# Kernel optimization log

Measured on AMD Instinct MI355X. Metric: run time of the kernel, lower is better.

## Reference

```python
import jax, jax.numpy as jnp
import numpy as np

H, D = 6, 64          # num_heads, head_dim (embed_dim = 384)
WIN = 33              # window_size
PAD = (WIN - 1) // 2  # 16


def setup_inputs() -> dict:
    key = jax.random.key(0)
    ks = jax.random.split(key, 9)
    B, L, E = 8, 1025, 384
    s = 1.0 / np.sqrt(E).astype(np.float32)
    return {
        "x": jax.random.normal(ks[0], (B, L, E), jnp.float32),
        "Wq": jax.random.normal(ks[1], (E, E), jnp.float32) * s,
        "bq": jax.random.normal(ks[2], (E,), jnp.float32) * 0.01,
        "Wk": jax.random.normal(ks[3], (E, E), jnp.float32) * s,
        "bk": jax.random.normal(ks[4], (E,), jnp.float32) * 0.01,
        "Wv": jax.random.normal(ks[5], (E, E), jnp.float32) * s,
        "bv": jax.random.normal(ks[6], (E,), jnp.float32) * 0.01,
        "Wo": jax.random.normal(ks[7], (E, E), jnp.float32) * s,
        "bo": jax.random.normal(ks[8], (E,), jnp.float32) * 0.01,
    }


def reference(x, Wq, bq, Wk, bk, Wv, bv, Wo, bo):
    B, L, E = x.shape
    scale = 1.0 / np.sqrt(D).astype(np.float32)

    def proj(W, b):
        # (B,L,E) -> (B,H,L,D)
        return (x @ W + b).reshape(B, L, H, D).transpose(0, 2, 1, 3)

    Q, K, V = proj(Wq, bq), proj(Wk, bk), proj(Wv, bv)

    # --- cls token (position 0): full attention over all keys ---
    s_cls = jnp.einsum('bhqd,bhkd->bhqk', Q[:, :, :1], K) * scale
    out_cls = jnp.einsum('bhqk,bhkd->bhqd', jax.nn.softmax(s_cls, -1), V)

    # --- remaining tokens: local window + cls appended to every window ---
    Lr = L - 1
    pos = jnp.arange(1, L)                                    # absolute query pos (Lr,)
    idx = pos[:, None] + jnp.arange(WIN)[None, :] - PAD
    # original masks out-of-range AND the cls slot (abs pos 0) inside the window
    valid = (idx >= 1) & (idx < L)
    idxc = jnp.clip(idx, 0, L - 1)

    Kw = K[:, :, idxc]
    Vw = V[:, :, idxc]
    cls_k = jnp.broadcast_to(K[:, :, :1, None, :], (B, H, Lr, 1, D))
    cls_v = jnp.broadcast_to(V[:, :, :1, None, :], (B, H, Lr, 1, D))
    Kw = jnp.concatenate([Kw, cls_k], axis=3)
    Vw = jnp.concatenate([Vw, cls_v], axis=3)
    mask = jnp.concatenate([valid, jnp.ones((Lr, 1), bool)], axis=-1)

    s_rest = jnp.einsum('bhld,bhlwd->bhlw', Q[:, :, 1:], Kw) * scale
    s_rest = jnp.where(mask[None, None], s_rest, -jnp.inf)
    a_rest = jax.nn.softmax(s_rest, axis=-1)
    out_rest = jnp.einsum('bhlw,bhlwd->bhld', a_rest, Vw)

    out = jnp.concatenate([out_cls, out_rest], axis=2)        # (B,H,L,D)
    out = out.transpose(0, 2, 1, 3).reshape(B, L, E)
    return out @ Wo + bo
```

## Files before the change

kernel.cpp:

```cpp
#include <hip/hip_runtime.h>
#include <hip/hip_bf16.h>

typedef unsigned short ushort_t;
typedef __attribute__((ext_vector_type(8))) short short8;
typedef __attribute__((ext_vector_type(4))) float f32x4;

constexpr int Bc = 8;
constexpr int Lc = 1025;
constexpr int Ec = 384;
constexpr int Hc = 6;
constexpr int Dc = 64;
constexpr int MT = Bc * Lc;
constexpr int BHLD = Bc * Hc * Lc * Dc;
constexpr float SCALE = 0.125f;
constexpr int NCH = 5;

__device__ __forceinline__ float bf2f(ushort_t u) {
    union { unsigned int u; float f; } v; v.u = ((unsigned int)u) << 16; return v.f;
}
__device__ __forceinline__ ushort_t f2bf(float f) {
    union { float f; unsigned int u; } v; v.f = f;
    unsigned int r = v.u + 0x7FFFu + ((v.u >> 16) & 1u);
    return (ushort_t)(r >> 16);
}

#define GLOAD_LDS16(gp, lp)                                                          \
    __builtin_amdgcn_global_load_lds(                                                \
        (const __attribute__((address_space(1))) unsigned int*)(gp),                 \
        (__attribute__((address_space(3))) unsigned int*)(lp), 16, 0, 0)

__global__ __launch_bounds__(256) void prep_kernel(
    const float* __restrict__ x, ushort_t* __restrict__ xb,
    const float* __restrict__ Wq, const float* __restrict__ Wk,
    const float* __restrict__ Wv, const float* __restrict__ Wo,
    ushort_t* __restrict__ Wt_all)
{
    const int bid = blockIdx.x;
    if (bid < 3075) {
        int i = bid * 256 + threadIdx.x;
        float4 v = ((const float4*)x)[i];
        ushort4 o;
        o.x = f2bf(v.x); o.y = f2bf(v.y); o.z = f2bf(v.z); o.w = f2bf(v.w);
        ((ushort4*)xb)[i] = o;
        return;
    }
    __shared__ float t[32][33];
    const int b2 = bid - 3075;
    const int z = b2 / 144, rem = b2 - z * 144;
    const int yy = rem / 12, xx = rem - yy * 12;
    const float* W = (z == 0) ? Wq : (z == 1) ? Wk : (z == 2) ? Wv : Wo;
    ushort_t* Wt = Wt_all + (size_t)z * Ec * Ec;
    const int x0 = xx * 32, y0 = yy * 32;
    const int tx = threadIdx.x & 31, ty = threadIdx.x >> 5;
#pragma unroll
    for (int j = 0; j < 4; j++)
        t[ty + 8 * j][tx] = W[(size_t)(y0 + ty + 8 * j) * Ec + x0 + tx];
    __syncthreads();
#pragma unroll
    for (int j = 0; j < 4; j++)
        Wt[(size_t)(x0 + ty + 8 * j) * Ec + y0 + tx] = f2bf(t[tx][ty + 8 * j]);
}

__global__ __launch_bounds__(256) void qkv_mfma_kernel(
    const ushort_t* __restrict__ xb, const ushort_t* __restrict__ Wt,
    const float* __restrict__ bq, const float* __restrict__ bk,
    const float* __restrict__ bv, ushort_t* __restrict__ qkv)
{
    __shared__ __align__(16) ushort_t Asm[64 * 384];
    __shared__ __align__(16) ushort_t Bsm[2][128 * 64];

    const int tid = threadIdx.x;
    const int lane = tid & 63;
    const int wid = tid >> 6;
    const int wr = wid & 1, wc = wid >> 1;
    const int m0 = blockIdx.x * 64;
    const int which = blockIdx.y;
    const ushort_t* Wmat = Wt + (size_t)which * Ec * Ec;
    const float* bias = (which == 0) ? bq : (which == 1) ? bk : bv;
    ushort_t* outp = qkv + (size_t)which * BHLD;

#pragma unroll
    for (int i = 0; i < 12; i++) {
        int wchunk = wid * 12 + i;
        int ci = wchunk * 64 + lane;
        int row = ci / 48, c = ci - row * 48;
        int cg = (c & ~7) | ((c & 7) ^ (row & 7));
        int rowA = m0 + row; rowA = rowA < MT ? rowA : MT - 1;
        GLOAD_LDS16(xb + (size_t)rowA * Ec + cg * 8,
                    Asm + (size_t)wchunk * 512);
    }

#define B_STAGE(S, BUF)                                                          \
    {                                                                            \
        int ns_ = (S) / 6, kt_ = (S) - ns_ * 6;                                  \
        _Pragma("unroll")                                                        \
        for (int c = 0; c < 4; c++) {                                            \
            int ci  = (wid * 4 + c) * 64 + lane;                                 \
            int row = ci >> 3, kc = ci & 7;                                      \
            int kcs = kc ^ (row & 7);                                            \
            GLOAD_LDS16(Wmat + (size_t)(ns_ * 128 + row) * Ec + kt_ * 64 + kcs * 8, \
                        Bsm[BUF] + (size_t)(wid * 4 + c) * 512);                 \
        }                                                                        \
    }

    B_STAGE(0, 0);
    B_STAGE(1, 1);

    f32x4 acc[2][4];
#pragma unroll
    for (int i = 0; i < 2; i++)
#pragma unroll
        for (int j = 0; j < 4; j++) acc[i][j] = (f32x4){0.f, 0.f, 0.f, 0.f};

    const int colL = lane & 15;
    const int rowL = (lane >> 4) * 4;

    for (int s = 0; s < 18; ++s) {
        const int cb = s & 1;
        const int ns = s / 6, kt = s - ns * 6;
        if (s < 17) { asm volatile("s_waitcnt vmcnt(4)" ::: "memory"); }
        else        { asm volatile("s_waitcnt vmcnt(0)" ::: "memory"); }
        __builtin_amdgcn_sched_barrier(0);
        __builtin_amdgcn_s_barrier();

        short8 a[2][2], b[2][4];
#pragma unroll
        for (int ki = 0; ki < 2; ki++) {
            const int kc = ki * 4 + (lane >> 4);
#pragma unroll
            for (int mi = 0; mi < 2; mi++) {
                int row = wr * 32 + mi * 16 + (lane & 15);
                a[ki][mi] = *(const short8*)(
                    Asm + row * 384 + (kt * 8 + (kc ^ (row & 7))) * 8);
            }
#pragma unroll
            for (int ni = 0; ni < 4; ni++) {
                int row = wc * 64 + ni * 16 + (lane & 15);
                b[ki][ni] = *(const short8*)(
                    Bsm[cb] + row * 64 + ((kc ^ (row & 7)) * 8));
            }
        }
        asm volatile("s_waitcnt lgkmcnt(0)" ::: "memory");
        __builtin_amdgcn_sched_barrier(0);
        __builtin_amdgcn_s_barrier();

        if (s + 2 < 18) B_STAGE(s + 2, cb);

#pragma unroll
        for (int ki = 0; ki < 2; ki++)
#pragma unroll
            for (int mi = 0; mi < 2; mi++)
#pragma unroll
                for (int ni = 0; ni < 4; ni++)
                    acc[mi][ni] = __builtin_amdgcn_mfma_f32_16x16x32_bf16(
                        a[ki][mi], b[ki][ni], acc[mi][ni], 0, 0, 0);

        if (kt == 5) {
#pragma unroll
            for (int ni = 0; ni < 4; ni++) {
                int nm = ns * 128 + wc * 64 + ni * 16 + colL;
                float bv_ = bias[nm];
                int h = nm >> 6, d = nm & 63;
#pragma unroll
                for (int mi = 0; mi < 2; mi++) {
#pragma unroll
                    for (int r = 0; r < 4; r++) {
                        int m = m0 + wr * 32 + mi * 16 + rowL + r;
                        if (m < MT) {
                            int b_ = m / Lc, l = m - b_ * Lc;
                            outp[((size_t)(b_ * Hc + h) * Lc + l) * Dc + d] =
                                f2bf(acc[mi][ni][r] + bv_);
                        }
                    }
                    acc[mi][ni] = (f32x4){0.f, 0.f, 0.f, 0.f};
                }
            }
        }
    }
#undef B_STAGE
}

__global__ __launch_bounds__(256) void cls_part_kernel(
    const ushort_t* __restrict__ qkv, float* __restrict__ part)
{
    const int bh = blockIdx.x, ch = blockIdx.y;
    const int base = ch * 256;
    const int count = min(256, Lc - base);
    const ushort_t* Q = qkv + (size_t)bh * Lc * Dc;
    const ushort_t* K = Q + (size_t)BHLD;
    const ushort_t* V = Q + 2 * (size_t)BHLD;

    __shared__ float qs[64];
    __shared__ float ps[256];
    __shared__ float red[256];

    const int tid = threadIdx.x;
    if (tid < 64) qs[tid] = bf2f(Q[tid]);
    __syncthreads();

    float s = -1e30f;
    if (tid < count) {
        const ushort4* kp = (const ushort4*)(K + (size_t)(base + tid) * Dc);
        float acc = 0.f;
#pragma unroll
        for (int c = 0; c < 16; c++) {
            ushort4 kv = kp[c];
            acc += qs[c * 4 + 0] * bf2f(kv.x) + qs[c * 4 + 1] * bf2f(kv.y) +
                   qs[c * 4 + 2] * bf2f(kv.z) + qs[c * 4 + 3] * bf2f(kv.w);
        }
        s = acc * SCALE;
    }
    red[tid] = s; __syncthreads();
    for (int off = 128; off > 0; off >>= 1) {
        if (tid < off) red[tid] = fmaxf(red[tid], red[tid + off]);
        __syncthreads();
    }
    const float m = red[0];
    __syncthreads();

    float p = (tid < count) ? __expf(s - m) : 0.f;
    ps[tid] = p;
    red[tid] = p; __syncthreads();
    for (int off = 128; off > 0; off >>= 1) {
        if (tid < off) red[tid] += red[tid + off];
        __syncthreads();
    }
    const float S = red[0];
    __syncthreads();

    const int d = tid & 63, sl = tid >> 6;
    float acc = 0.f;
    for (int i = sl; i < count; i += 4)
        acc += ps[i] * bf2f(V[(size_t)(base + i) * Dc + d]);
    red[tid] = acc; __syncthreads();
    if (tid < 64) {
        float o = red[tid] + red[tid + 64] + red[tid + 128] + red[tid + 192];
        float* pp = part + (size_t)(bh * NCH + ch) * 66;
        pp[2 + tid] = o;
        if (tid == 0) { pp[0] = m; pp[1] = S; }
    }
}

__global__ __launch_bounds__(256) void win_attn_kernel(
    const ushort_t* __restrict__ qkv, const float* __restrict__ part,
    ushort_t* __restrict__ attnb)
{
    __shared__ __align__(16) ushort_t Kb[128 * 64];
    __shared__ __align__(16) ushort_t Vb[64 * 128];
    __shared__ __align__(16) ushort_t QP[64 * 128];

    const int bh = blockIdx.y;
    const int tid = threadIdx.x, lane = tid & 63, wid = tid >> 6;
    const int b_ = bh / Hc, h = bh - b_ * Hc;

    if (blockIdx.x == 16) {
        if (tid >= 64) return;
        float M = -1e30f;
#pragma unroll
        for (int ch = 0; ch < NCH; ch++)
            M = fmaxf(M, part[(size_t)(bh * NCH + ch) * 66]);
        float S = 0.f, O = 0.f;
#pragma unroll
        for (int ch = 0; ch < NCH; ch++) {
            const float* pp = part + (size_t)(bh * NCH + ch) * 66;
            float w = __expf(pp[0] - M);
            S += pp[1] * w;
            O += pp[2 + tid] * w;
        }
        attnb[(size_t)(b_ * Lc) * Ec + h * 64 + tid] = f2bf(O / S);
        return;
    }

    const int t = blockIdx.x;
    const int l0 = 1 + t * 64;
    const int k0n = l0 - 16;
    const ushort_t* Qg = qkv + (size_t)bh * Lc * Dc;
    const ushort_t* Kg = Qg + (size_t)BHLD;
    const ushort_t* Vg = Qg + 2 * (size_t)BHLD;

    short8 vreg[4];
    int vrow[4], vdc[4];
#pragma unroll
    for (int i = 0; i < 4; i++) {
        int ci = i * 256 + tid;
        if (ci < 896) {
            int j = ci >> 3, dc = ci & 7;
            int kp = (j <= 95) ? min(max(k0n + j, 0), 1024) : 0;
            vreg[i] = *(const short8*)(Vg + (size_t)kp * Dc + dc * 8);
            vrow[i] = j; vdc[i] = dc;
        } else { vrow[i] = -1; vdc[i] = 0; }
    }

#pragma unroll
    for (int i = 0; i < 4; i++) {
        int wchunk = i * 4 + wid;
        if (wchunk < 14) {
            int p = wchunk * 64 + lane;
            int j = p >> 3, c = p & 7, g = c ^ (j & 7);
            int kp = (j <= 95) ? min(max(k0n + j, 0), 1024) : 0;
            GLOAD_LDS16(Kg + (size_t)kp * Dc + g * 8,
                        Kb + (size_t)wchunk * 512);
        }
    }
#pragma unroll
    for (int i = 0; i < 2; i++) {
        int p = (i * 4 + wid) * 64 + lane;
        int q = p >> 3, c = p & 7, g = c ^ (q & 7);
        GLOAD_LDS16(Qg + (size_t)(l0 + q) * Dc + g * 8,
                    QP + (size_t)(i * 4 + wid) * 512);
    }

#pragma unroll
    for (int i = 0; i < 4; i++) {
        if (vrow[i] >= 0) {
            int j = vrow[i], jc3 = j >> 3, j7 = j & 7;
#pragma unroll
            for (int z = 0; z < 8; z++) {
                int d = vdc[i] * 8 + z;
                Vb[d * 128 + ((jc3 ^ (d & 15)) * 8) + j7] = (ushort_t)vreg[i][z];
            }
        }
    }
    if (tid < 128) {
        int d = tid >> 1, lcn = 14 + (tid & 1);
        *(short8*)(Vb + d * 128 + ((lcn ^ (d & 15)) * 8)) =
            (short8){0, 0, 0, 0, 0, 0, 0, 0};
    }
    __syncthreads();

    f32x4 sacc[7];
#pragma unroll
    for (int tj = 0; tj < 7; tj++) sacc[tj] = (f32x4){0.f, 0.f, 0.f, 0.f};
#pragma unroll
    for (int ki = 0; ki < 2; ki++) {
        const int gc = ki * 4 + (lane >> 4);
        const int qrow = wid * 16 + (lane & 15);
        short8 a = *(const short8*)(QP + qrow * 64 + ((gc ^ (qrow & 7)) * 8));
#pragma unroll
        for (int tj = 0; tj < 7; tj++) {
            int jrow = tj * 16 + (lane & 15);
            short8 b = *(const short8*)(Kb + jrow * 64 + ((gc ^ (jrow & 7)) * 8));
            sacc[tj] = __builtin_amdgcn_mfma_f32_16x16x32_bf16(a, b, sacc[tj], 0, 0, 0);
        }
    }
    __syncthreads();

    const int qb = wid * 16 + (lane >> 4) * 4;
    const int cl = lane & 15;
    float inv[4];
#pragma unroll
    for (int r = 0; r < 4; r++) {
        const int q = qb + r;
        float sv[7];
        float mx = -1e30f;
#pragma unroll
        for (int tj = 0; tj < 7; tj++) {
            int j = tj * 16 + cl;
            int kp = k0n + j;
            bool valid = (j == 96) ||
                         ((j >= q) && (j <= q + 32) && (kp >= 1) && (kp <= 1024));
            float s = valid ? sacc[tj][r] * SCALE : -1e30f;
            sv[tj] = s;
            mx = fmaxf(mx, s);
        }
        mx = fmaxf(mx, __shfl_xor(mx, 1));
        mx = fmaxf(mx, __shfl_xor(mx, 2));
        mx = fmaxf(mx, __shfl_xor(mx, 4));
        mx = fmaxf(mx, __shfl_xor(mx, 8));
        float sum = 0.f;
#pragma unroll
        for (int tj = 0; tj < 7; tj++) {
            float pv = __expf(sv[tj] - mx);
            sv[tj] = pv;
            sum += pv;
        }
        sum += __shfl_xor(sum, 1);
        sum += __shfl_xor(sum, 2);
        sum += __shfl_xor(sum, 4);
        sum += __shfl_xor(sum, 8);
        inv[r] = 1.f / sum;
#pragma unroll
        for (int tj = 0; tj < 7; tj++) {
            int j = tj * 16 + cl;
            QP[q * 128 + (((j >> 3) ^ (q & 15)) * 8) + (j & 7)] = f2bf(sv[tj]);
        }
    }
    if (cl == 0) {
#pragma unroll
        for (int r = 0; r < 4; r++) {
            int q = qb + r;
            *(short8*)(QP + q * 128 + ((14 ^ (q & 15)) * 8)) =
                (short8){0, 0, 0, 0, 0, 0, 0, 0};
            *(short8*)(QP + q * 128 + ((15 ^ (q & 15)) * 8)) =
                (short8){0, 0, 0, 0, 0, 0, 0, 0};
        }
    }
    __syncthreads();

    f32x4 oacc[4];
#pragma unroll
    for (int dt = 0; dt < 4; dt++) oacc[dt] = (f32x4){0.f, 0.f, 0.f, 0.f};
#pragma unroll
    for (int kc = 0; kc < 4; kc++) {
        const int gc = kc * 4 + (lane >> 4);
        const int qrow = wid * 16 + (lane & 15);
        short8 pa = *(const short8*)(QP + qrow * 128 + ((gc ^ (qrow & 15)) * 8));
#pragma unroll
        for (int dt = 0; dt < 4; dt++) {
            int drow = dt * 16 + (lane & 15);
            short8 vb = *(const short8*)(Vb + drow * 128 + ((gc ^ (drow & 15)) * 8));
            oacc[dt] = __builtin_amdgcn_mfma_f32_16x16x32_bf16(pa, vb, oacc[dt], 0, 0, 0);
        }
    }

#pragma unroll
    for (int dt = 0; dt < 4; dt++) {
        int d = dt * 16 + cl;
#pragma unroll
        for (int r = 0; r < 4; r++) {
            int l = l0 + qb + r;
            attnb[(size_t)(b_ * Lc + l) * Ec + h * 64 + d] = f2bf(oacc[dt][r] * inv[r]);
        }
    }
}

__global__ __launch_bounds__(256) void out_mfma_kernel(
    const ushort_t* __restrict__ attn_rows, const ushort_t* __restrict__ Wot,
    const float* __restrict__ bo, float* __restrict__ out)
{
    __shared__ __align__(16) ushort_t As[2][64 * 64];
    __shared__ __align__(16) ushort_t Bs[2][128 * 64];

    const int tid = threadIdx.x;
    const int lane = tid & 63;
    const int wid = tid >> 6;
    const int wr = wid & 1, wc = wid >> 1;
    const int m0 = blockIdx.x * 64;
    const int n0 = blockIdx.y * 128;

    f32x4 acc[2][4];
#pragma unroll
    for (int i = 0; i < 2; i++)
#pragma unroll
        for (int j = 0; j < 4; j++) acc[i][j] = (f32x4){0.f, 0.f, 0.f, 0.f};

#define OUT_STAGE(KT, BUF)                                                       \
    {                                                                            \
        _Pragma("unroll")                                                        \
        for (int c = 0; c < 2; c++) {                                            \
            int ci  = (wid * 2 + c) * 64 + lane;                                 \
            int row = ci >> 3, kc = ci & 7;                                      \
            int kcs = kc ^ (row & 7);                                            \
            int rowA = m0 + row; rowA = rowA < MT ? rowA : MT - 1;               \
            GLOAD_LDS16(attn_rows + (size_t)rowA * Ec + (KT) + kcs * 8,          \
                        As[BUF] + (size_t)(wid * 2 + c) * 512);                  \
        }                                                                        \
        _Pragma("unroll")                                                        \
        for (int c = 0; c < 4; c++) {                                            \
            int ci  = (wid * 4 + c) * 64 + lane;                                 \
            int row = ci >> 3, kc = ci & 7;                                      \
            int kcs = kc ^ (row & 7);                                            \
            GLOAD_LDS16(Wot + (size_t)(n0 + row) * Ec + (KT) + kcs * 8,          \
                        Bs[BUF] + (size_t)(wid * 4 + c) * 512);                  \
        }                                                                        \
    }

    OUT_STAGE(0, 0);
    OUT_STAGE(64, 1);

    for (int t = 0; t < 6; ++t) {
        const int cb = t & 1;
        if (t < 5) { asm volatile("s_waitcnt vmcnt(6)" ::: "memory"); }
        else       { asm volatile("s_waitcnt vmcnt(0)" ::: "memory"); }
        __builtin_amdgcn_sched_barrier(0);
        __builtin_amdgcn_s_barrier();

        short8 a[2][2], b[2][4];
#pragma unroll
        for (int ki = 0; ki < 2; ki++) {
            const int kchunk = ki * 4 + (lane >> 4);
#pragma unroll
            for (int mi = 0; mi < 2; mi++) {
                int row = wr * 32 + mi * 16 + (lane & 15);
                a[ki][mi] = *(const short8*)(As[cb] + row * 64 + ((kchunk ^ (row & 7)) * 8));
            }
#pragma unroll
            for (int ni = 0; ni < 4; ni++) {
                int row = wc * 64 + ni * 16 + (lane & 15);
                b[ki][ni] = *(const short8*)(Bs[cb] + row * 64 + ((kchunk ^ (row & 7)) * 8));
            }
        }
        asm volatile("s_waitcnt lgkmcnt(0)" ::: "memory");
        __builtin_amdgcn_sched_barrier(0);
        __builtin_amdgcn_s_barrier();

        if (t + 2 < 6) OUT_STAGE((t + 2) * 64, cb);

#pragma unroll
        for (int ki = 0; ki < 2; ki++)
#pragma unroll
            for (int mi = 0; mi < 2; mi++)
#pragma unroll
                for (int ni = 0; ni < 4; ni++)
                    acc[mi][ni] = __builtin_amdgcn_mfma_f32_16x16x32_bf16(
                        a[ki][mi], b[ki][ni], acc[mi][ni], 0, 0, 0);
    }
#undef OUT_STAGE

    const int colL = lane & 15;
    const int rowL = (lane >> 4) * 4;
#pragma unroll
    for (int ni = 0; ni < 4; ni++) {
        int n = n0 + wc * 64 + ni * 16 + colL;
        float bo_v = bo[n];
#pragma unroll
        for (int mi = 0; mi < 2; mi++) {
#pragma unroll
            for (int r = 0; r < 4; r++) {
                int m = m0 + wr * 32 + mi * 16 + rowL + r;
                if (m < MT) out[(size_t)m * Ec + n] = acc[mi][ni][r] + bo_v;
            }
        }
    }
}

extern "C" void kernel_launch(void* const* d_in, const int* in_sizes, int n_in,
                              void* d_out, int out_size, void* d_ws, size_t ws_size,
                              hipStream_t stream)
{
    const float* x  = (const float*)d_in[0];
    const float* Wq = (const float*)d_in[1];
    const float* bq = (const float*)d_in[2];
    const float* Wk = (const float*)d_in[3];
    const float* bk = (const float*)d_in[4];
    const float* Wv = (const float*)d_in[5];
    const float* bv = (const float*)d_in[6];
    const float* Wo = (const float*)d_in[7];
    const float* bo = (const float*)d_in[8];
    float* out = (float*)d_out;

    ushort_t* xb    = (ushort_t*)d_ws;
    ushort_t* Wt    = xb + (size_t)MT * Ec;
    ushort_t* qkvb  = Wt + (size_t)4 * Ec * Ec;
    ushort_t* attnb = qkvb + (size_t)3 * BHLD;
    float* clsp     = (float*)(attnb + (size_t)MT * Ec);

    prep_kernel<<<3075 + 576, 256, 0, stream>>>(x, xb, Wq, Wk, Wv, Wo, Wt);

    qkv_mfma_kernel<<<dim3((MT + 63) / 64, 3), 256, 0, stream>>>(
        xb, Wt, bq, bk, bv, qkvb);

    cls_part_kernel<<<dim3(Bc * Hc, NCH), 256, 0, stream>>>(qkvb, clsp);

    win_attn_kernel<<<dim3(17, Bc * Hc), 256, 0, stream>>>(qkvb, clsp, attnb);

    out_mfma_kernel<<<dim3((MT + 63) / 64, 3), 256, 0, stream>>>(
        attnb, Wt + (size_t)3 * Ec * Ec, bo, out);
}
```

Baseline: 160.3 us.

## Fuse all stages into one persistent cooperative kernel with grid syncs

Replaces five separate kernel launches (prep, QKV GEMM, cls partials, window attention, output GEMM) with one cooperative persistent kernel that walks each stage's jobs in a grid-stride loop and separates stages with grid.sync(). Shared memory comes from one 80 KB pool that each stage reinterprets. The aim is to remove launch gaps and per-kernel tail effects. In exchange, grid-wide barriers add cost, the grid is capped at 512 blocks, and the large LDS pool and register pressure may limit occupancy for the GEMM and attention phases.

```diff
diff --git a/kernel.cpp b/kernel.cpp
--- a/kernel.cpp
+++ b/kernel.cpp
@@ -1,5 +1,8 @@
 #include <hip/hip_runtime.h>
 #include <hip/hip_bf16.h>
+#include <hip/hip_cooperative_groups.h>
+
+namespace cg = cooperative_groups;
 
 typedef unsigned short ushort_t;
 typedef __attribute__((ext_vector_type(8))) short short8;
@@ -29,66 +32,74 @@
         (const __attribute__((address_space(1))) unsigned int*)(gp),                 \
         (__attribute__((address_space(3))) unsigned int*)(lp), 16, 0, 0)
 
-__global__ __launch_bounds__(256) void prep_kernel(
-    const float* __restrict__ x, ushort_t* __restrict__ xb,
+__global__ __launch_bounds__(256, 2) void fused_kernel(
+    const float* __restrict__ x,
     const float* __restrict__ Wq, const float* __restrict__ Wk,
     const float* __restrict__ Wv, const float* __restrict__ Wo,
-    ushort_t* __restrict__ Wt_all)
+    const float* __restrict__ bq, const float* __restrict__ bk,
+    const float* __restrict__ bv, const float* __restrict__ bo,
+    ushort_t* __restrict__ xb, ushort_t* __restrict__ Wt_all,
+    ushort_t* __restrict__ qkvb, float* __restrict__ clsp,
+    ushort_t* __restrict__ attnb, float* __restrict__ out)
 {
-    const int bid = blockIdx.x;
-    if (bid < 3075) {
-        int i = bid * 256 + threadIdx.x;
-        float4 v = ((const float4*)x)[i];
-        ushort4 o;
-        o.x = f2bf(v.x); o.y = f2bf(v.y); o.z = f2bf(v.z); o.w = f2bf(v.w);
-        ((ushort4*)xb)[i] = o;
-        return;
-    }
-    __shared__ float t[32][33];
-    const int b2 = bid - 3075;
-    const int z = b2 / 144, rem = b2 - z * 144;
-    const int yy = rem / 12, xx = rem - yy * 12;
-    const float* W = (z == 0) ? Wq : (z == 1) ? Wk : (z == 2) ? Wv : Wo;
-    ushort_t* Wt = Wt_all + (size_t)z * Ec * Ec;
-    const int x0 = xx * 32, y0 = yy * 32;
-    const int tx = threadIdx.x & 31, ty = threadIdx.x >> 5;
-#pragma unroll
-    for (int j = 0; j < 4; j++)
-        t[ty + 8 * j][tx] = W[(size_t)(y0 + ty + 8 * j) * Ec + x0 + tx];
-    __syncthreads();
-#pragma unroll
-    for (int j = 0; j < 4; j++)
-        Wt[(size_t)(x0 + ty + 8 * j) * Ec + y0 + tx] = f2bf(t[tx][ty + 8 * j]);
-}
-
-__global__ __launch_bounds__(256) void qkv_mfma_kernel(
-    const ushort_t* __restrict__ xb, const ushort_t* __restrict__ Wt,
-    const float* __restrict__ bq, const float* __restrict__ bk,
-    const float* __restrict__ bv, ushort_t* __restrict__ qkv)
-{
-    __shared__ __align__(16) ushort_t Asm[64 * 384];
-    __shared__ __align__(16) ushort_t Bsm[2][128 * 64];
-
+    __shared__ __align__(16) unsigned char POOL[81920];
+
+    cg::grid_group grid = cg::this_grid();
+    const int nb  = gridDim.x;
+    const int bx  = blockIdx.x;
     const int tid = threadIdx.x;
     const int lane = tid & 63;
-    const int wid = tid >> 6;
-    const int wr = wid & 1, wc = wid >> 1;
-    const int m0 = blockIdx.x * 64;
-    const int which = blockIdx.y;
-    const ushort_t* Wmat = Wt + (size_t)which * Ec * Ec;
-    const float* bias = (which == 0) ? bq : (which == 1) ? bk : bv;
-    ushort_t* outp = qkv + (size_t)which * BHLD;
-
-#pragma unroll
-    for (int i = 0; i < 12; i++) {
-        int wchunk = wid * 12 + i;
-        int ci = wchunk * 64 + lane;
-        int row = ci / 48, c = ci - row * 48;
-        int cg = (c & ~7) | ((c & 7) ^ (row & 7));
-        int rowA = m0 + row; rowA = rowA < MT ? rowA : MT - 1;
-        GLOAD_LDS16(xb + (size_t)rowA * Ec + cg * 8,
-                    Asm + (size_t)wchunk * 512);
-    }
+    const int wid  = tid >> 6;
+
+    for (int job = bx; job < 3075 + 576; job += nb) {
+        if (job < 3075) {
+            int i = job * 256 + tid;
+            float4 v = ((const float4*)x)[i];
+            ushort4 o;
+            o.x = f2bf(v.x); o.y = f2bf(v.y); o.z = f2bf(v.z); o.w = f2bf(v.w);
+            ((ushort4*)xb)[i] = o;
+        } else {
+            float (*t)[33] = (float (*)[33])POOL;
+            const int b2 = job - 3075;
+            const int z = b2 / 144, rem = b2 - z * 144;
+            const int yy = rem / 12, xx = rem - yy * 12;
+            const float* W = (z == 0) ? Wq : (z == 1) ? Wk : (z == 2) ? Wv : Wo;
+            ushort_t* Wt = Wt_all + (size_t)z * Ec * Ec;
+            const int x0 = xx * 32, y0 = yy * 32;
+            const int tx = tid & 31, ty = tid >> 5;
+#pragma unroll
+            for (int j = 0; j < 4; j++)
+                t[ty + 8 * j][tx] = W[(size_t)(y0 + ty + 8 * j) * Ec + x0 + tx];
+            __syncthreads();
+#pragma unroll
+            for (int j = 0; j < 4; j++)
+                Wt[(size_t)(x0 + ty + 8 * j) * Ec + y0 + tx] = f2bf(t[tx][ty + 8 * j]);
+            __syncthreads();
+        }
+    }
+    grid.sync();
+
+    for (int job = bx; job < 129 * 3; job += nb) {
+        ushort_t* Asm = (ushort_t*)POOL;
+        ushort_t* BsmB = (ushort_t*)(POOL + 49152);
+
+        const int wr = wid & 1, wc = wid >> 1;
+        const int m0 = (job % 129) * 64;
+        const int which = job / 129;
+        const ushort_t* Wmat = Wt_all + (size_t)which * Ec * Ec;
+        const float* bias = (which == 0) ? bq : (which == 1) ? bk : bv;
+        ushort_t* outp = qkvb + (size_t)which * BHLD;
+
+#pragma unroll
+        for (int i = 0; i < 12; i++) {
+            int wchunk = wid * 12 + i;
+            int ci = wchunk * 64 + lane;
+            int row = ci / 48, c = ci - row * 48;
+            int cg_ = (c & ~7) | ((c & 7) ^ (row & 7));
+            int rowA = m0 + row; rowA = rowA < MT ? rowA : MT - 1;
+            GLOAD_LDS16(xb + (size_t)rowA * Ec + cg_ * 8,
+                        Asm + (size_t)wchunk * 512);
+        }
 
 #define B_STAGE(S, BUF)                                                          \
     {                                                                            \
@@ -99,350 +110,345 @@
             int row = ci >> 3, kc = ci & 7;                                      \
             int kcs = kc ^ (row & 7);                                            \
             GLOAD_LDS16(Wmat + (size_t)(ns_ * 128 + row) * Ec + kt_ * 64 + kcs * 8, \
-                        Bsm[BUF] + (size_t)(wid * 4 + c) * 512);                 \
+                        BsmB + (size_t)(BUF) * 8192 + (size_t)(wid * 4 + c) * 512); \
         }                                                                        \
     }
 
-    B_STAGE(0, 0);
-    B_STAGE(1, 1);
-
-    f32x4 acc[2][4];
-#pragma unroll
-    for (int i = 0; i < 2; i++)
-#pragma unroll
-        for (int j = 0; j < 4; j++) acc[i][j] = (f32x4){0.f, 0.f, 0.f, 0.f};
-
-    const int colL = lane & 15;
-    const int rowL = (lane >> 4) * 4;
-
-    for (int s = 0; s < 18; ++s) {
-        const int cb = s & 1;
-        const int ns = s / 6, kt = s - ns * 6;
-        if (s < 17) { asm volatile("s_waitcnt vmcnt(4)" ::: "memory"); }
-        else        { asm volatile("s_waitcnt vmcnt(0)" ::: "memory"); }
-        __builtin_amdgcn_sched_barrier(0);
-        __builtin_amdgcn_s_barrier();
-
-        short8 a[2][2], b[2][4];
+        B_STAGE(0, 0);
+        B_STAGE(1, 1);
+
+        f32x4 acc[2][4];
+#pragma unroll
+        for (int i = 0; i < 2; i++)
+#pragma unroll
+            for (int j = 0; j < 4; j++) acc[i][j] = (f32x4){0.f, 0.f, 0.f, 0.f};
+
+        const int colL = lane & 15;
+        const int rowL = (lane >> 4) * 4;
+
+        for (int s = 0; s < 18; ++s) {
+            const int cb = s & 1;
+            const int ns = s / 6, kt = s - ns * 6;
+            if (s < 17) { asm volatile("s_waitcnt vmcnt(4)" ::: "memory"); }
+            else        { asm volatile("s_waitcnt vmcnt(0)" ::: "memory"); }
+            __builtin_amdgcn_sched_barrier(0);
+            __builtin_amdgcn_s_barrier();
+
+            short8 a[2][2], b[2][4];
+#pragma unroll
+            for (int ki = 0; ki < 2; ki++) {
+                const int kc = ki * 4 + (lane >> 4);
+#pragma unroll
+                for (int mi = 0; mi < 2; mi++) {
+                    int row = wr * 32 + mi * 16 + (lane & 15);
+                    a[ki][mi] = *(const short8*)(
+                        Asm + row * 384 + (kt * 8 + (kc ^ (row & 7))) * 8);
+                }
+#pragma unroll
+                for (int ni = 0; ni < 4; ni++) {
+                    int row = wc * 64 + ni * 16 + (lane & 15);
+                    b[ki][ni] = *(const short8*)(
+                        BsmB + (size_t)cb * 8192 + row * 64 + ((kc ^ (row & 7)) * 8));
+                }
+            }
+            asm volatile("s_waitcnt lgkmcnt(0)" ::: "memory");
+            __builtin_amdgcn_sched_barrier(0);
+            __builtin_amdgcn_s_barrier();
+
+            if (s + 2 < 18) B_STAGE(s + 2, cb);
+
+#pragma unroll
+            for (int ki = 0; ki < 2; ki++)
+#pragma unroll
+                for (int mi = 0; mi < 2; mi++)
+#pragma unroll
+                    for (int ni = 0; ni < 4; ni++)
+                        acc[mi][ni] = __builtin_amdgcn_mfma_f32_16x16x32_bf16(
+                            a[ki][mi], b[ki][ni], acc[mi][ni], 0, 0, 0);
+
+            if (kt == 5) {
+#pragma unroll
+                for (int ni = 0; ni < 4; ni++) {
+                    int nm = ns * 128 + wc * 64 + ni * 16 + colL;
+                    float bv_ = bias[nm];
+                    int h = nm >> 6, d = nm & 63;
+#pragma unroll
+                    for (int mi = 0; mi < 2; mi++) {
+#pragma unroll
+                        for (int r = 0; r < 4; r++) {
+                            int m = m0 + wr * 32 + mi * 16 + rowL + r;
+                            if (m < MT) {
+                                int b_ = m / Lc, l = m - b_ * Lc;
+                                outp[((size_t)(b_ * Hc + h) * Lc + l) * Dc + d] =
+                                    f2bf(acc[mi][ni][r] + bv_);
+                            }
+                        }
+                        acc[mi][ni] = (f32x4){0.f, 0.f, 0.f, 0.f};
+                    }
+                }
+            }
+        }
+#undef B_STAGE
+    }
+    grid.sync();
+
+    for (int job = bx; job < Bc * Hc * NCH; job += nb) {
+        float* qs  = (float*)POOL;
+        float* ps  = qs + 64;
+        float* red = ps + 256;
+
+        const int bh = job / NCH, ch = job - bh * NCH;
+        const int base = ch * 256;
+        const int count = min(256, Lc - base);
+        const ushort_t* Q = qkvb + (size_t)bh * Lc * Dc;
+        const ushort_t* K = Q + (size_t)BHLD;
+        const ushort_t* V = Q + 2 * (size_t)BHLD;
+
+        if (tid < 64) qs[tid] = bf2f(Q[tid]);
+        __syncthreads();
+
+        float s = -1e30f;
+        if (tid < count) {
+            const ushort4* kp = (const ushort4*)(K + (size_t)(base + tid) * Dc);
+            float acc = 0.f;
+#pragma unroll
+            for (int c = 0; c < 16; c++) {
+                ushort4 kv = kp[c];
+                acc += qs[c * 4 + 0] * bf2f(kv.x) + qs[c * 4 + 1] * bf2f(kv.y) +
+                       qs[c * 4 + 2] * bf2f(kv.z) + qs[c * 4 + 3] * bf2f(kv.w);
+            }
+            s = acc * SCALE;
+        }
+        red[tid] = s; __syncthreads();
+        for (int off = 128; off > 0; off >>= 1) {
+            if (tid < off) red[tid] = fmaxf(red[tid], red[tid + off]);
+            __syncthreads();
+        }
+        const float m = red[0];
+        __syncthreads();
+
+        float p = (tid < count) ? __expf(s - m) : 0.f;
+        ps[tid] = p;
+        red[tid] = p; __syncthreads();
+        for (int off = 128; off > 0; off >>= 1) {
+            if (tid < off) red[tid] += red[tid + off];
+            __syncthreads();
+        }
+        const float S = red[0];
+        __syncthreads();
+
+        const int d = tid & 63, sl = tid >> 6;
+        float acc = 0.f;
+        for (int i = sl; i < count; i += 4)
+            acc += ps[i] * bf2f(V[(size_t)(base + i) * Dc + d]);
+        red[tid] = acc; __syncthreads();
+        if (tid < 64) {
+            float o = red[tid] + red[tid + 64] + red[tid + 128] + red[tid + 192];
+            float* pp = clsp + (size_t)(bh * NCH + ch) * 66;
+            pp[2 + tid] = o;
+            if (tid == 0) { pp[0] = m; pp[1] = S; }
+        }
+        __syncthreads();
+    }
+    grid.sync();
+
+    for (int job = bx; job < 768 + 48; job += nb) {
+        __syncthreads();
+
+        if (job >= 768) {
+            const int bh = job - 768;
+            const int b_ = bh / Hc, h = bh - b_ * Hc;
+            if (tid < 64) {
+                float M = -1e30f;
+#pragma unroll
+                for (int ch = 0; ch < NCH; ch++)
+                    M = fmaxf(M, clsp[(size_t)(bh * NCH + ch) * 66]);
+                float S = 0.f, O = 0.f;
+#pragma unroll
+                for (int ch = 0; ch < NCH; ch++) {
+                    const float* pp = clsp + (size_t)(bh * NCH + ch) * 66;
+                    float w = __expf(pp[0] - M);
+                    S += pp[1] * w;
+                    O += pp[2 + tid] * w;
+                }
+                attnb[(size_t)(b_ * Lc) * Ec + h * 64 + tid] = f2bf(O / S);
+            }
+            continue;
+        }
+
+        ushort_t* Kb = (ushort_t*)POOL;
+        ushort_t* Vb = (ushort_t*)(POOL + 16384);
+        ushort_t* QP = (ushort_t*)(POOL + 32768);
+
+        const int t = job % 16, bh = job / 16;
+        const int b_ = bh / Hc, h = bh - b_ * Hc;
+        const int l0 = 1 + t * 64;
+        const int k0n = l0 - 16;
+        const ushort_t* Qg = qkvb + (size_t)bh * Lc * Dc;
+        const ushort_t* Kg = Qg + (size_t)BHLD;
+        const ushort_t* Vg = Qg + 2 * (size_t)BHLD;
+
+        short8 vreg[4];
+        int vrow[4], vdc[4];
+#pragma unroll
+        for (int i = 0; i < 4; i++) {
+            int ci = i * 256 + tid;
+            if (ci < 896) {
+                int j = ci >> 3, dc = ci & 7;
+                int kp = (j <= 95) ? min(max(k0n + j, 0), 1024) : 0;
+                vreg[i] = *(const short8*)(Vg + (size_t)kp * Dc + dc * 8);
+                vrow[i] = j; vdc[i] = dc;
+            } else { vrow[i] = -1; vdc[i] = 0; }
+        }
+
+#pragma unroll
+        for (int i = 0; i < 4; i++) {
+            int wchunk = i * 4 + wid;
+            if (wchunk < 14) {
+                int p = wchunk * 64 + lane;
+                int j = p >> 3, c = p & 7, g = c ^ (j & 7);
+                int kp = (j <= 95) ? min(max(k0n + j, 0), 1024) : 0;
+                GLOAD_LDS16(Kg + (size_t)kp * Dc + g * 8,
+                            Kb + (size_t)wchunk * 512);
+            }
+        }
+#pragma unroll
+        for (int i = 0; i < 2; i++) {
+            int p = (i * 4 + wid) * 64 + lane;
+            int q = p >> 3, c = p & 7, g = c ^ (q & 7);
+            GLOAD_LDS16(Qg + (size_t)(l0 + q) * Dc + g * 8,
+                        QP + (size_t)(i * 4 + wid) * 512);
+        }
+
+#pragma unroll
+        for (int i = 0; i < 4; i++) {
+            if (vrow[i] >= 0) {
+                int j = vrow[i], jc3 = j >> 3, j7 = j & 7;
+#pragma unroll
+                for (int z = 0; z < 8; z++) {
+                    int d = vdc[i] * 8 + z;
+                    Vb[d * 128 + ((jc3 ^ (d & 15)) * 8) + j7] = (ushort_t)vreg[i][z];
+                }
+            }
+        }
+        if (tid < 128) {
+            int d = tid >> 1, lcn = 14 + (tid & 1);
+            *(short8*)(Vb + d * 128 + ((lcn ^ (d & 15)) * 8)) =
+                (short8){0, 0, 0, 0, 0, 0, 0, 0};
+        }
+        __syncthreads();
+
+        f32x4 sacc[7];
+#pragma unroll
+        for (int tj = 0; tj < 7; tj++) sacc[tj] = (f32x4){0.f, 0.f, 0.f, 0.f};
 #pragma unroll
         for (int ki = 0; ki < 2; ki++) {
-            const int kc = ki * 4 + (lane >> 4);
-#pragma unroll
-            for (int mi = 0; mi < 2; mi++) {
-                int row = wr * 32 + mi * 16 + (lane & 15);
-                a[ki][mi] = *(const short8*)(
-                    Asm + row * 384 + (kt * 8 + (kc ^ (row & 7))) * 8);
-            }
-#pragma unroll
-            for (int ni = 0; ni < 4; ni++) {
-                int row = wc * 64 + ni * 16 + (lane & 15);
-                b[ki][ni] = *(const short8*)(
-                    Bsm[cb] + row * 64 + ((kc ^ (row & 7)) * 8));
-            }
-        }
-        asm volatile("s_waitcnt lgkmcnt(0)" ::: "memory");
-        __builtin_amdgcn_sched_barrier(0);
-        __builtin_amdgcn_s_barrier();
-
-        if (s + 2 < 18) B_STAGE(s + 2, cb);
-
-#pragma unroll
-        for (int ki = 0; ki < 2; ki++)
-#pragma unroll
-            for (int mi = 0; mi < 2; mi++)
-#pragma unroll
-                for (int ni = 0; ni < 4; ni++)
-                    acc[mi][ni] = __builtin_amdgcn_mfma_f32_16x16x32_bf16(
-                        a[ki][mi], b[ki][ni], acc[mi][ni], 0, 0, 0);
-
-        if (kt == 5) {
-#pragma unroll
-            for (int ni = 0; ni < 4; ni++) {
-                int nm = ns * 128 + wc * 64 + ni * 16 + colL;
-                float bv_ = bias[nm];
-                int h = nm >> 6, d = nm & 63;
-#pragma unroll
-                for (int mi = 0; mi < 2; mi++) {
-#pragma unroll
-                    for (int r = 0; r < 4; r++) {
-                        int m = m0 + wr * 32 + mi * 16 + rowL + r;
-                        if (m < MT) {
-                            int b_ = m / Lc, l = m - b_ * Lc;
-                            outp[((size_t)(b_ * Hc + h) * Lc + l) * Dc + d] =
-                                f2bf(acc[mi][ni][r] + bv_);
-                        }
-                    }
-                    acc[mi][ni] = (f32x4){0.f, 0.f, 0.f, 0.f};
-                }
-            }
-        }
-    }
-#undef B_STAGE
-}
-
-__global__ __launch_bounds__(256) void cls_part_kernel(
-    const ushort_t* __restrict__ qkv, float* __restrict__ part)
-{
-    const int bh = blockIdx.x, ch = blockIdx.y;
-    const int base = ch * 256;
-    const int count = min(256, Lc - base);
-    const ushort_t* Q = qkv + (size_t)bh * Lc * Dc;
-    const ushort_t* K = Q + (size_t)BHLD;
-    const ushort_t* V = Q + 2 * (size_t)BHLD;
-
-    __shared__ float qs[64];
-    __shared__ float ps[256];
-    __shared__ float red[256];
-
-    const int tid = threadIdx.x;
-    if (tid < 64) qs[tid] = bf2f(Q[tid]);
-    __syncthreads();
-
-    float s = -1e30f;
-    if (tid < count) {
-        const ushort4* kp = (const ushort4*)(K + (size_t)(base + tid) * Dc);
-        float acc = 0.f;
-#pragma unroll
-        for (int c = 0; c < 16; c++) {
-            ushort4 kv = kp[c];
-            acc += qs[c * 4 + 0] * bf2f(kv.x) + qs[c * 4 + 1] * bf2f(kv.y) +
-                   qs[c * 4 + 2] * bf2f(kv.z) + qs[c * 4 + 3] * bf2f(kv.w);
-        }
-        s = acc * SCALE;
-    }
-    red[tid] = s; __syncthreads();
-    for (int off = 128; off > 0; off >>= 1) {
-        if (tid < off) red[tid] = fmaxf(red[tid], red[tid + off]);
-        __syncthreads();
-    }
-    const float m = red[0];
-    __syncthreads();
-
-    float p = (tid < count) ? __expf(s - m) : 0.f;
-    ps[tid] = p;
-    red[tid] = p; __syncthreads();
-    for (int off = 128; off > 0; off >>= 1) {
-        if (tid < off) red[tid] += red[tid + off];
-        __syncthreads();
-    }
-    const float S = red[0];
-    __syncthreads();
-
-    const int d = tid & 63, sl = tid >> 6;
-    float acc = 0.f;
-    for (int i = sl; i < count; i += 4)
-        acc += ps[i] * bf2f(V[(size_t)(base + i) * Dc + d]);
-    red[tid] = acc; __syncthreads();
-    if (tid < 64) {
-        float o = red[tid] + red[tid + 64] + red[tid + 128] + red[tid + 192];
-        float* pp = part + (size_t)(bh * NCH + ch) * 66;
-        pp[2 + tid] = o;
-        if (tid == 0) { pp[0] = m; pp[1] = S; }
-    }
-}
-
-__global__ __launch_bounds__(256) void win_attn_kernel(
-    const ushort_t* __restrict__ qkv, const float* __restrict__ part,
-    ushort_t* __restrict__ attnb)
-{
-    __shared__ __align__(16) ushort_t Kb[128 * 64];
-    __shared__ __align__(16) ushort_t Vb[64 * 128];
-    __shared__ __align__(16) ushort_t QP[64 * 128];
-
-    const int bh = blockIdx.y;
-    const int tid = threadIdx.x, lane = tid & 63, wid = tid >> 6;
-    const int b_ = bh / Hc, h = bh - b_ * Hc;
-
-    if (blockIdx.x == 16) {
-        if (tid >= 64) return;
-        float M = -1e30f;
-#pragma unroll
-        for (int ch = 0; ch < NCH; ch++)
-            M = fmaxf(M, part[(size_t)(bh * NCH + ch) * 66]);
-        float S = 0.f, O = 0.f;
-#pragma unroll
-        for (int ch = 0; ch < NCH; ch++) {
-            const float* pp = part + (size_t)(bh * NCH + ch) * 66;
-            float w = __expf(pp[0] - M);
-            S += pp[1] * w;
-            O += pp[2 + tid] * w;
-        }
-        attnb[(size_t)(b_ * Lc) * Ec + h * 64 + tid] = f2bf(O / S);
-        return;
-    }
-
-    const int t = blockIdx.x;
-    const int l0 = 1 + t * 64;
-    const int k0n = l0 - 16;
-    const ushort_t* Qg = qkv + (size_t)bh * Lc * Dc;
-    const ushort_t* Kg = Qg + (size_t)BHLD;
-    const ushort_t* Vg = Qg + 2 * (size_t)BHLD;
-
-    short8 vreg[4];
-    int vrow[4], vdc[4];
-#pragma unroll
-    for (int i = 0; i < 4; i++) {
-        int ci = i * 256 + tid;
-        if (ci < 896) {
-            int j = ci >> 3, dc = ci & 7;
-            int kp = (j <= 95) ? min(max(k0n + j, 0), 1024) : 0;
-            vreg[i] = *(const short8*)(Vg + (size_t)kp * Dc + dc * 8);
-            vrow[i] = j; vdc[i] = dc;
-        } else { vrow[i] = -1; vdc[i] = 0; }
-    }
-
-#pragma unroll
-    for (int i = 0; i < 4; i++) {
-        int wchunk = i * 4 + wid;
-        if (wchunk < 14) {
-            int p = wchunk * 64 + lane;
-            int j = p >> 3, c = p & 7, g = c ^ (j & 7);
-            int kp = (j <= 95) ? min(max(k0n + j, 0), 1024) : 0;
-            GLOAD_LDS16(Kg + (size_t)kp * Dc + g * 8,
-                        Kb + (size_t)wchunk * 512);
-        }
-    }
-#pragma unroll
-    for (int i = 0; i < 2; i++) {
-        int p = (i * 4 + wid) * 64 + lane;
-        int q = p >> 3, c = p & 7, g = c ^ (q & 7);
-        GLOAD_LDS16(Qg + (size_t)(l0 + q) * Dc + g * 8,
-                    QP + (size_t)(i * 4 + wid) * 512);
-    }
-
-#pragma unroll
-    for (int i = 0; i < 4; i++) {
-        if (vrow[i] >= 0) {
-            int j = vrow[i], jc3 = j >> 3, j7 = j & 7;
-#pragma unroll
-            for (int z = 0; z < 8; z++) {
-                int d = vdc[i] * 8 + z;
-                Vb[d * 128 + ((jc3 ^ (d & 15)) * 8) + j7] = (ushort_t)vreg[i][z];
-            }
-        }
-    }
-    if (tid < 128) {
-        int d = tid >> 1, lcn = 14 + (tid & 1);
-        *(short8*)(Vb + d * 128 + ((lcn ^ (d & 15)) * 8)) =
-            (short8){0, 0, 0, 0, 0, 0, 0, 0};
-    }
-    __syncthreads();
-
-    f32x4 sacc[7];
-#pragma unroll
-    for (int tj = 0; tj < 7; tj++) sacc[tj] = (f32x4){0.f, 0.f, 0.f, 0.f};
-#pragma unroll
-    for (int ki = 0; ki < 2; ki++) {
-        const int gc = ki * 4 + (lane >> 4);
-        const int qrow = wid * 16 + (lane & 15);
-        short8 a = *(const short8*)(QP + qrow * 64 + ((gc ^ (qrow & 7)) * 8));
-#pragma unroll
-        for (int tj = 0; tj < 7; tj++) {
-            int jrow = tj * 16 + (lane & 15);
-            short8 b = *(const short8*)(Kb + jrow * 64 + ((gc ^ (jrow & 7)) * 8));
-            sacc[tj] = __builtin_amdgcn_mfma_f32_16x16x32_bf16(a, b, sacc[tj], 0, 0, 0);
-        }
-    }
-    __syncthreads();
-
-    const int qb = wid * 16 + (lane >> 4) * 4;
-    const int cl = lane & 15;
-    float inv[4];
-#pragma unroll
-    for (int r = 0; r < 4; r++) {
-        const int q = qb + r;
-        float sv[7];
-        float mx = -1e30f;
-#pragma unroll
-        for (int tj = 0; tj < 7; tj++) {
-            int j = tj * 16 + cl;
-            int kp = k0n + j;
-            bool valid = (j == 96) ||
-                         ((j >= q) && (j <= q + 32) && (kp >= 1) && (kp <= 1024));
-            float s = valid ? sacc[tj][r] * SCALE : -1e30f;
-            sv[tj] = s;
-            mx = fmaxf(mx, s);
-        }
-        mx = fmaxf(mx, __shfl_xor(mx, 1));
-        mx = fmaxf(mx, __shfl_xor(mx, 2));
-        mx = fmaxf(mx, __shfl_xor(mx, 4));
-        mx = fmaxf(mx, __shfl_xor(mx, 8));
-        float sum = 0.f;
-#pragma unroll
-        for (int tj = 0; tj < 7; tj++) {
-            float pv = __expf(sv[tj] - mx);
-            sv[tj] = pv;
-            sum += pv;
-        }
-        sum += __shfl_xor(sum, 1);
-        sum += __shfl_xor(sum, 2);
-        sum += __shfl_xor(sum, 4);
-        sum += __shfl_xor(sum, 8);
-        inv[r] = 1.f / sum;
-#pragma unroll
-        for (int tj = 0; tj < 7; tj++) {
-            int j = tj * 16 + cl;
-            QP[q * 128 + (((j >> 3) ^ (q & 15)) * 8) + (j & 7)] = f2bf(sv[tj]);
-        }
-    }
-    if (cl == 0) {
+            const int gc = ki * 4 + (lane >> 4);
+            const int qrow = wid * 16 + (lane & 15);
+            short8 a = *(const short8*)(QP + qrow * 64 + ((gc ^ (qrow & 7)) * 8));
+#pragma unroll
+            for (int tj = 0; tj < 7; tj++) {
+                int jrow = tj * 16 + (lane & 15);
+                short8 b = *(const short8*)(Kb + jrow * 64 + ((gc ^ (jrow & 7)) * 8));
+                sacc[tj] = __builtin_amdgcn_mfma_f32_16x16x32_bf16(a, b, sacc[tj], 0, 0, 0);
+            }
+        }
+        __syncthreads();
+
+        const int qb = wid * 16 + (lane >> 4) * 4;
+        const int cl = lane & 15;
+        float inv[4];
 #pragma unroll
         for (int r = 0; r < 4; r++) {
-            int q = qb + r;
-            *(short8*)(QP + q * 128 + ((14 ^ (q & 15)) * 8)) =
-                (short8){0, 0, 0, 0, 0, 0, 0, 0};
-            *(short8*)(QP + q * 128 + ((15 ^ (q & 15)) * 8)) =
-                (short8){0, 0, 0, 0, 0, 0, 0, 0};
-        }
-    }
-    __syncthreads();
-
-    f32x4 oacc[4];
-#pragma unroll
-    for (int dt = 0; dt < 4; dt++) oacc[dt] = (f32x4){0.f, 0.f, 0.f, 0.f};
-#pragma unroll
-    for (int kc = 0; kc < 4; kc++) {
-        const int gc = kc * 4 + (lane >> 4);
-        const int qrow = wid * 16 + (lane & 15);
-        short8 pa = *(const short8*)(QP + qrow * 128 + ((gc ^ (qrow & 15)) * 8));
+            const int q = qb + r;
+            float sv[7];
+            float mx = -1e30f;
+#pragma unroll
+            for (int tj = 0; tj < 7; tj++) {
+                int j = tj * 16 + cl;
+                int kp = k0n + j;
+                bool valid = (j == 96) ||
+                             ((j >= q) && (j <= q + 32) && (kp >= 1) && (kp <= 1024));
+                float s = valid ? sacc[tj][r] * SCALE : -1e30f;
+                sv[tj] = s;
+                mx = fmaxf(mx, s);
+            }
+            mx = fmaxf(mx, __shfl_xor(mx, 1));
+            mx = fmaxf(mx, __shfl_xor(mx, 2));
+            mx = fmaxf(mx, __shfl_xor(mx, 4));
+            mx = fmaxf(mx, __shfl_xor(mx, 8));
+            float sum = 0.f;
+#pragma unroll
+            for (int tj = 0; tj < 7; tj++) {
+                float pv = __expf(sv[tj] - mx);
+                sv[tj] = pv;
+                sum += pv;
+            }
+            sum += __shfl_xor(sum, 1);
+            sum += __shfl_xor(sum, 2);
+            sum += __shfl_xor(sum, 4);
+            sum += __shfl_xor(sum, 8);
+            inv[r] = 1.f / sum;
+#pragma unroll
+            for (int tj = 0; tj < 7; tj++) {
+                int j = tj * 16 + cl;
+                QP[q * 128 + (((j >> 3) ^ (q & 15)) * 8) + (j & 7)] = f2bf(sv[tj]);
+            }
+        }
+        if (cl == 0) {
+#pragma unroll
+            for (int r = 0; r < 4; r++) {
+                int q = qb + r;
+                *(short8*)(QP + q * 128 + ((14 ^ (q & 15)) * 8)) =
+                    (short8){0, 0, 0, 0, 0, 0, 0, 0};
+                *(short8*)(QP + q * 128 + ((15 ^ (q & 15)) * 8)) =
+                    (short8){0, 0, 0, 0, 0, 0, 0, 0};
+            }
+        }
+        __syncthreads();
+
+        f32x4 oacc[4];
+#pragma unroll
+        for (int dt = 0; dt < 4; dt++) oacc[dt] = (f32x4){0.f, 0.f, 0.f, 0.f};
+#pragma unroll
+        for (int kc = 0; kc < 4; kc++) {
+            const int gc = kc * 4 + (lane >> 4);
+            const int qrow = wid * 16 + (lane & 15);
+            short8 pa = *(const short8*)(QP + qrow * 128 + ((gc ^ (qrow & 15)) * 8));
+#pragma unroll
+            for (int dt = 0; dt < 4; dt++) {
+                int drow = dt * 16 + (lane & 15);
+                short8 vb = *(const short8*)(Vb + drow * 128 + ((gc ^ (drow & 15)) * 8));
+                oacc[dt] = __builtin_amdgcn_mfma_f32_16x16x32_bf16(pa, vb, oacc[dt], 0, 0, 0);
+            }
+        }
+
 #pragma unroll
         for (int dt = 0; dt < 4; dt++) {
-            int drow = dt * 16 + (lane & 15);
-            short8 vb = *(const short8*)(Vb + drow * 128 + ((gc ^ (drow & 15)) * 8));
-            oacc[dt] = __builtin_amdgcn_mfma_f32_16x16x32_bf16(pa, vb, oacc[dt], 0, 0, 0);
-        }
-    }
-
-#pragma unroll
-    for (int dt = 0; dt < 4; dt++) {
-        int d = dt * 16 + cl;
-#pragma unroll
-        for (int r = 0; r < 4; r++) {
-            int l = l0 + qb + r;
-            attnb[(size_t)(b_ * Lc + l) * Ec + h * 64 + d] = f2bf(oacc[dt][r] * inv[r]);
-        }
-    }
-}
-
-__global__ __launch_bounds__(256) void out_mfma_kernel(
-    const ushort_t* __restrict__ attn_rows, const ushort_t* __restrict__ Wot,
-    const float* __restrict__ bo, float* __restrict__ out)
-{
-    __shared__ __align__(16) ushort_t As[2][64 * 64];
-    __shared__ __align__(16) ushort_t Bs[2][128 * 64];
-
-    const int tid = threadIdx.x;
-    const int lane = tid & 63;
-    const int wid = tid >> 6;
-    const int wr = wid & 1, wc = wid >> 1;
-    const int m0 = blockIdx.x * 64;
-    const int n0 = blockIdx.y * 128;
-
-    f32x4 acc[2][4];
-#pragma unroll
-    for (int i = 0; i < 2; i++)
-#pragma unroll
-        for (int j = 0; j < 4; j++) acc[i][j] = (f32x4){0.f, 0.f, 0.f, 0.f};
+            int d = dt * 16 + cl;
+#pragma unroll
+            for (int r = 0; r < 4; r++) {
+                int l = l0 + qb + r;
+                attnb[(size_t)(b_ * Lc + l) * Ec + h * 64 + d] = f2bf(oacc[dt][r] * inv[r]);
+            }
+        }
+    }
+    grid.sync();
+
+    for (int job = bx; job < 129 * 3; job += nb) {
+        ushort_t* AsB = (ushort_t*)POOL;
+        ushort_t* BsB = (ushort_t*)(POOL + 16384);
+        const ushort_t* Wot = Wt_all + (size_t)3 * Ec * Ec;
+
+        const int wr = wid & 1, wc = wid >> 1;
+        const int m0 = (job % 129) * 64;
+        const int n0 = (job / 129) * 128;
+
+        f32x4 acc[2][4];
+#pragma unroll
+        for (int i = 0; i < 2; i++)
+#pragma unroll
+            for (int j = 0; j < 4; j++) acc[i][j] = (f32x4){0.f, 0.f, 0.f, 0.f};
 
 #define OUT_STAGE(KT, BUF)                                                       \
     {                                                                            \
@@ -452,8 +458,8 @@
             int row = ci >> 3, kc = ci & 7;                                      \
             int kcs = kc ^ (row & 7);                                            \
             int rowA = m0 + row; rowA = rowA < MT ? rowA : MT - 1;               \
-            GLOAD_LDS16(attn_rows + (size_t)rowA * Ec + (KT) + kcs * 8,          \
-                        As[BUF] + (size_t)(wid * 2 + c) * 512);                  \
+            GLOAD_LDS16(attnb + (size_t)rowA * Ec + (KT) + kcs * 8,              \
+                        AsB + (size_t)(BUF) * 4096 + (size_t)(wid * 2 + c) * 512); \
         }                                                                        \
         _Pragma("unroll")                                                        \
         for (int c = 0; c < 4; c++) {                                            \
@@ -461,64 +467,67 @@
             int row = ci >> 3, kc = ci & 7;                                      \
             int kcs = kc ^ (row & 7);                                            \
             GLOAD_LDS16(Wot + (size_t)(n0 + row) * Ec + (KT) + kcs * 8,          \
-                        Bs[BUF] + (size_t)(wid * 4 + c) * 512);                  \
+                        BsB + (size_t)(BUF) * 8192 + (size_t)(wid * 4 + c) * 512); \
         }                                                                        \
     }
 
-    OUT_STAGE(0, 0);
-    OUT_STAGE(64, 1);
-
-    for (int t = 0; t < 6; ++t) {
-        const int cb = t & 1;
-        if (t < 5) { asm volatile("s_waitcnt vmcnt(6)" ::: "memory"); }
-        else       { asm volatile("s_waitcnt vmcnt(0)" ::: "memory"); }
-        __builtin_amdgcn_sched_barrier(0);
-        __builtin_amdgcn_s_barrier();
-
-        short8 a[2][2], b[2][4];
-#pragma unroll
-        for (int ki = 0; ki < 2; ki++) {
-            const int kchunk = ki * 4 + (lane >> 4);
+        OUT_STAGE(0, 0);
+        OUT_STAGE(64, 1);
+
+        for (int s = 0; s < 6; ++s) {
+            const int cb = s & 1;
+            if (s < 5) { asm volatile("s_waitcnt vmcnt(6)" ::: "memory"); }
+            else       { asm volatile("s_waitcnt vmcnt(0)" ::: "memory"); }
+            __builtin_amdgcn_sched_barrier(0);
+            __builtin_amdgcn_s_barrier();
+
+            short8 a[2][2], b[2][4];
+#pragma unroll
+            for (int ki = 0; ki < 2; ki++) {
+                const int kchunk = ki * 4 + (lane >> 4);
+#pragma unroll
+                for (int mi = 0; mi < 2; mi++) {
+                    int row = wr * 32 + mi * 16 + (lane & 15);
+                    a[ki][mi] = *(const short8*)(
+                        AsB + (size_t)cb * 4096 + row * 64 + ((kchunk ^ (row & 7)) * 8));
+                }
+#pragma unroll
+                for (int ni = 0; ni < 4; ni++) {
+                    int row = wc * 64 + ni * 16 + (lane & 15);
+                    b[ki][ni] = *(const short8*)(
+                        BsB + (size_t)cb * 8192 + row * 64 + ((kchunk ^ (row & 7)) * 8));
+                }
+            }
+            asm volatile("s_waitcnt lgkmcnt(0)" ::: "memory");
+            __builtin_amdgcn_sched_barrier(0);
+            __builtin_amdgcn_s_barrier();
+
+            if (s + 2 < 6) OUT_STAGE((s + 2) * 64, cb);
+
+#pragma unroll
+            for (int ki = 0; ki < 2; ki++)
+#pragma unroll
+                for (int mi = 0; mi < 2; mi++)
+#pragma unroll
+                    for (int ni = 0; ni < 4; ni++)
+                        acc[mi][ni] = __builtin_amdgcn_mfma_f32_16x16x32_bf16(
+                            a[ki][mi], b[ki][ni], acc[mi][ni], 0, 0, 0);
+        }
+#undef OUT_STAGE
+
+        const int colL = lane & 15;
+        const int rowL = (lane >> 4) * 4;
+#pragma unroll
+        for (int ni = 0; ni < 4; ni++) {
+            int n = n0 + wc * 64 + ni * 16 + colL;
+            float bo_v = bo[n];
 #pragma unroll
             for (int mi = 0; mi < 2; mi++) {
-                int row = wr * 32 + mi * 16 + (lane & 15);
-                a[ki][mi] = *(const short8*)(As[cb] + row * 64 + ((kchunk ^ (row & 7)) * 8));
-            }
-#pragma unroll
-            for (int ni = 0; ni < 4; ni++) {
-                int row = wc * 64 + ni * 16 + (lane & 15);
-                b[ki][ni] = *(const short8*)(Bs[cb] + row * 64 + ((kchunk ^ (row & 7)) * 8));
-            }
-        }
-        asm volatile("s_waitcnt lgkmcnt(0)" ::: "memory");
-        __builtin_amdgcn_sched_barrier(0);
-        __builtin_amdgcn_s_barrier();
-
-        if (t + 2 < 6) OUT_STAGE((t + 2) * 64, cb);
-
-#pragma unroll
-        for (int ki = 0; ki < 2; ki++)
-#pragma unroll
-            for (int mi = 0; mi < 2; mi++)
-#pragma unroll
-                for (int ni = 0; ni < 4; ni++)
-                    acc[mi][ni] = __builtin_amdgcn_mfma_f32_16x16x32_bf16(
-                        a[ki][mi], b[ki][ni], acc[mi][ni], 0, 0, 0);
-    }
-#undef OUT_STAGE
-
-    const int colL = lane & 15;
-    const int rowL = (lane >> 4) * 4;
-#pragma unroll
-    for (int ni = 0; ni < 4; ni++) {
-        int n = n0 + wc * 64 + ni * 16 + colL;
-        float bo_v = bo[n];
-#pragma unroll
-        for (int mi = 0; mi < 2; mi++) {
-#pragma unroll
-            for (int r = 0; r < 4; r++) {
-                int m = m0 + wr * 32 + mi * 16 + rowL + r;
-                if (m < MT) out[(size_t)m * Ec + n] = acc[mi][ni][r] + bo_v;
+#pragma unroll
+                for (int r = 0; r < 4; r++) {
+                    int m = m0 + wr * 32 + mi * 16 + rowL + r;
+                    if (m < MT) out[(size_t)m * Ec + n] = acc[mi][ni][r] + bo_v;
+                }
             }
         }
     }
@@ -545,15 +554,18 @@
     ushort_t* attnb = qkvb + (size_t)3 * BHLD;
     float* clsp     = (float*)(attnb + (size_t)MT * Ec);
 
-    prep_kernel<<<3075 + 576, 256, 0, stream>>>(x, xb, Wq, Wk, Wv, Wo, Wt);
-
-    qkv_mfma_kernel<<<dim3((MT + 63) / 64, 3), 256, 0, stream>>>(
-        xb, Wt, bq, bk, bv, qkvb);
-
-    cls_part_kernel<<<dim3(Bc * Hc, NCH), 256, 0, stream>>>(qkvb, clsp);
-
-    win_attn_kernel<<<dim3(17, Bc * Hc), 256, 0, stream>>>(qkvb, clsp, attnb);
-
-    out_mfma_kernel<<<dim3((MT + 63) / 64, 3), 256, 0, stream>>>(
-        attnb, Wt + (size_t)3 * Ec * Ec, bo, out);
+    int maxb = 0;
+    hipOccupancyMaxActiveBlocksPerMultiprocessor(&maxb, (const void*)fused_kernel, 256, 0);
+    if (maxb < 1) maxb = 1;
+    int nblocks = maxb * 256;
+    if (nblocks > 512) nblocks = 512;
+
+    void* args[] = {
+        (void*)&x, (void*)&Wq, (void*)&Wk, (void*)&Wv, (void*)&Wo,
+        (void*)&bq, (void*)&bk, (void*)&bv, (void*)&bo,
+        (void*)&xb, (void*)&Wt, (void*)&qkvb, (void*)&clsp, (void*)&attnb,
+        (void*)&out
+    };
+    hipLaunchCooperativeKernel((const void*)fused_kernel, dim3(nblocks), dim3(256),
+                               args, 0, stream);
 }
```

After: 314.3 us. 96.0% more time.
